# Performance work log

Hardware: AMD Instinct MI355X
Metric: run time of the kernel (lower is better)

The kernel has to match this reference:

```python
import jax, jax.numpy as jnp
import numpy as np

T, NC, NT, D, H, LBL = 8, 512, 512, 256, 8, 3
NBF = 1419  # performer default: int(256 * ln(256))
EPS = 1e-4


def setup_inputs() -> dict:
    key = jax.random.key(0)
    ks = jax.random.split(key, 16)
    rn = lambda i, shape, sc=1.0: jax.random.normal(ks[i], shape, dtype=jnp.float32) * sc
    w = 1.0 / np.sqrt(D)
    return {
        'x_ctx': rn(0, (T, NC, D)),
        'label_train': rn(1, (T, NC, LBL)),
        'x_tgt': rn(2, (T, NT, D)),
        # task_encoder: 3-layer MLP (256+label_dim -> 256 -> 256 -> 256), ReLU
        'W1': rn(3, (D + LBL, D), 1.0 / np.sqrt(D + LBL)), 'b1': jnp.zeros((D,), jnp.float32),
        'W2': rn(4, (D, D), w), 'b2': jnp.zeros((D,), jnp.float32),
        'W3': rn(5, (D, D), w), 'b3': jnp.zeros((D,), jnp.float32),
        # per-head projections (8 distinct 256->256 Linears each for k/v/q)
        'Wk': rn(6, (H, D, D), w), 'bk': jnp.zeros((H, D), jnp.float32),
        'Wv': rn(7, (H, D, D), w), 'bv': jnp.zeros((H, D), jnp.float32),
        'Wq': rn(8, (H, D, D), w), 'bq': jnp.zeros((H, D), jnp.float32),
        # output head-merge projection (8*256 -> 256) and mu (256 -> 256)
        'Wo': rn(9, (H * D, D), 1.0 / np.sqrt(H * D)), 'bo': jnp.zeros((D,), jnp.float32),
        'Wmu': rn(10, (D, D), w), 'bmu': jnp.zeros((D,), jnp.float32),
        # FAVOR+ random projection matrix [nb_features, dim_head]
        'proj': rn(11, (NBF, D)),
    }


def _softmax_kernel(data, proj, is_query):
    # Performer FAVOR+ positive softmax-kernel features. data: [t,h,n,d]
    dn = D ** -0.25
    ratio = NBF ** -0.5
    dd = jnp.einsum('thnd,fd->thnf', data * dn, proj)          # [t,h,n,F]
    diag = 0.5 * jnp.sum(data * data, axis=-1) * (dn * dn)      # [t,h,n]
    if is_query:
        m = jnp.max(dd, axis=-1, keepdims=True)
    else:
        m = jnp.max(dd, axis=(-2, -1), keepdims=True)
    return ratio * (jnp.exp(dd - diag[..., None] - m) + EPS)


def reference(x_ctx, label_train, x_tgt, W1, b1, W2, b2, W3, b3,
              Wk, bk, Wv, bv, Wq, bq, Wo, bo, Wmu, bmu, proj):
    # task_encoder MLP on [x_ctx, label]
    h = jax.nn.relu(jnp.concatenate([x_ctx, label_train], axis=-1) @ W1 + b1)
    h = jax.nn.relu(h @ W2 + b2)
    cf = jax.nn.relu(h @ W3 + b3)                               # context_features [t,Nc,D]
    # per-head full-width projections: k from x_ctx, v from context_features, q from x_tgt
    k = jnp.einsum('tnd,hde->thne', x_ctx, Wk) + bk[None, :, None, :]
    v = jnp.einsum('tnd,hde->thne', cf, Wv) + bv[None, :, None, :]
    q = jnp.einsum('tnd,hde->thne', x_tgt, Wq) + bq[None, :, None, :]
    # non-causal Performer linear attention
    qp = _softmax_kernel(q, proj, True)                         # [t,h,Nt,F]
    kp = _softmax_kernel(k, proj, False)                        # [t,h,Nc,F]
    ksum = jnp.sum(kp, axis=-2)                                 # [t,h,F]
    d_inv = 1.0 / jnp.einsum('thnf,thf->thn', qp, ksum)         # [t,h,Nt]
    ctx = jnp.einsum('thnf,thne->thfe', kp, v)                  # [t,h,F,D]
    out = jnp.einsum('thnf,thfe,thn->thne', qp, ctx, d_inv)     # [t,h,Nt,D]
    # torch: permute(0,2,3,1).view(t,Nt,-1) -> head index fastest-varying
    out = jnp.transpose(out, (0, 2, 3, 1)).reshape(out.shape[0], out.shape[2], -1)
    rep = out @ Wo + bo                                         # [t,Nt,D]
    return rep @ Wmu + bmu                                      # mu / sample_features
```

## Files before the change

### kernel.cpp

```cpp
#include <hip/hip_runtime.h>
#include <hip/hip_bf16.h>

typedef __hip_bfloat16 bf16;
typedef __attribute__((ext_vector_type(8))) short short8;
typedef __attribute__((ext_vector_type(4))) float f32x4;
typedef __attribute__((ext_vector_type(4))) unsigned short us4;
#define DEV __device__ __forceinline__

static constexpr int T_ = 8, NC = 512, NT = 512, D_ = 256, H_ = 8, NBF = 1419;
static constexpr int FT32 = 46;
static constexpr float EPS_ = 1e-4f;
static constexpr float DN = 0.25f;
static constexpr float DIAG_SC = 0.03125f;

DEV float bf2f(unsigned short u) { return __uint_as_float(((unsigned)u) << 16); }
DEV float tofloat(bf16 x) { return __bfloat162float(x); }
DEV unsigned short f2bu(float x) { bf16 h = __float2bfloat16(x); return *(unsigned short*)&h; }

DEV float ldx(const void* p, long i, int isb) {
  if (isb) return bf2f(((const unsigned short*)p)[i]);
  return ((const float*)p)[i];
}
DEV void stx(void* p, long i, float v, int isb) {
  if (isb) ((bf16*)p)[i] = __float2bfloat16(v);
  else     ((float*)p)[i] = v;
}

DEV void async_copy16(const void* g, void* lds) {
  __builtin_amdgcn_global_load_lds(
      (const __attribute__((address_space(1))) unsigned int*)g,
      (__attribute__((address_space(3))) unsigned int*)lds, 16, 0, 0);
}

__global__ __launch_bounds__(256)
void detect_dtype(const void* __restrict__ x, int* __restrict__ flag)
{
  __shared__ int bad;
  if (threadIdx.x == 0) bad = 0;
  __syncthreads();
  int mybad = 0;
  for (int j = 0; j < 16; j++) {
    long i = 2L * (threadIdx.x + 256L * j);
    unsigned short u = ((const unsigned short*)x)[i];
    int e = (u >> 7) & 0xff, mant = u & 0x7f;
    bool b = (e == 0xff) || (e >= 141) || (e <= 93 && !(e == 0 && mant == 0));
    mybad += b ? 1 : 0;
  }
  atomicAdd(&bad, mybad);
  __syncthreads();
  if (threadIdx.x == 0) *flag = (bad > 1024) ? 0 : 1;
}

__global__ __launch_bounds__(256)
void conv_proj(const void* __restrict__ proj, bf16* __restrict__ projB,
               const int* __restrict__ dtFlag)
{
  const int fl = *dtFlag;
  int f = blockIdx.x, t = threadIdx.x;
  float v = (f < NBF) ? ldx(proj, (long)f * 256 + t, fl) : 0.f;
  projB[(long)f * 256 + t] = __float2bfloat16(v);
}

__global__ __launch_bounds__(256)
void conv_bf16(const void* __restrict__ src, bf16* __restrict__ dst,
               const int* __restrict__ dtFlag)
{
  const int fl = *dtFlag;
  long i = (long)blockIdx.x * 256 + threadIdx.x;
  dst[i] = __float2bfloat16(ldx(src, i, fl));
}

__global__ __launch_bounds__(256)
void conv_wT(const void* __restrict__ Wk, const void* __restrict__ Wv,
             const void* __restrict__ Wq, const void* __restrict__ Wo,
             const void* __restrict__ W1, const void* __restrict__ W2,
             const void* __restrict__ W3, const void* __restrict__ Wmu,
             bf16* __restrict__ WkT, bf16* __restrict__ WvT,
             bf16* __restrict__ WqT, bf16* __restrict__ WoT,
             bf16* __restrict__ W1T, bf16* __restrict__ W2T,
             bf16* __restrict__ W3T, bf16* __restrict__ WmuT,
             const int* __restrict__ dtFlag)
{
  __shared__ float tile[32][33];
  const int fl = *dtFlag;
  const int kt = blockIdx.x, nt = blockIdx.y, z = blockIdx.z, t = threadIdx.x;
  const void* in; bf16* out; int K; int perm = 0; long off = 0;
  if (z < 8)        { in = Wk;  out = WkT;  K = 256; off = (long)z * 65536; }
  else if (z < 16)  { in = Wv;  out = WvT;  K = 256; off = (long)(z - 8) * 65536; }
  else if (z < 24)  { in = Wq;  out = WqT;  K = 256; off = (long)(z - 16) * 65536; }
  else if (z == 24) { in = Wo;  out = WoT;  K = 2048; perm = 1; }
  else if (z == 25) { in = W1;  out = W1T;  K = 256; }
  else if (z == 26) { in = W2;  out = W2T;  K = 256; }
  else if (z == 27) { in = W3;  out = W3T;  K = 256; }
  else              { in = Wmu; out = WmuT; K = 256; }
  if (K == 256 && kt >= 8) return;
  const int k0 = kt * 32, n0 = nt * 32;
  const int row = t >> 3, cb = (t & 7) * 4;
  {
    int kk = k0 + row;
    int krow = perm ? (((kk & 255) << 3) | (kk >> 8)) : kk;
#pragma unroll
    for (int j = 0; j < 4; j++)
      tile[row][cb + j] = ldx(in, off + (long)krow * 256 + n0 + cb + j, fl);
  }
  __syncthreads();
  us4 o;
#pragma unroll
  for (int j = 0; j < 4; j++) o[j] = f2bu(tile[cb + j][row]);
  *(us4*)(out + off + (long)(n0 + row) * K + k0 + cb) = o;
}

__global__ __launch_bounds__(256)
void init_zero(float* __restrict__ p)
{
  p[blockIdx.x * 256 + threadIdx.x] = 0.f;
}

__global__ __launch_bounds__(256)
void gemm_mfma(const bf16* __restrict__ A, const bf16* __restrict__ BT,
               const void* __restrict__ bias,
               void* __restrict__ C, int cMode, int epi, int cT,
               const int* __restrict__ dtFlag, float* __restrict__ diagOut,
               float* __restrict__ svOut,
               int M, int N, int K, long sA, int divA, long sB, int modB, long sBias)
{
  __shared__ alignas(16) bf16 As[2][64 * 64];
  __shared__ alignas(16) bf16 Bs[2][64 * 64];
  const int fl = *dtFlag;
  const int cB = (cMode == 2) ? fl : cMode;
  const int t = threadIdx.x;
  const int bz = blockIdx.z;
  const long aOff = (long)(bz / divA) * sA;
  const long bOff = (long)(bz % modB) * sB;
  const long biasOff = (long)(bz % modB) * sBias;
  const long cOff = (long)bz * (long)M * N;
  const int m0 = blockIdx.y * 64, n0 = blockIdx.x * 64;
  const int w = t >> 6, l = t & 63, quad = l >> 4, ln = l & 15;
  const bf16* Ab = A + aOff + (long)m0 * K;
  const bf16* Bb = BT + bOff + (long)n0 * K;
  const int srow = l >> 3;
  const int scc = (l & 7) ^ srow;
  f32x4 acc[4] = {};

  auto stage = [&](int buf, int k0) {
#pragma unroll
    for (int j = 0; j < 2; j++) {
      const int rbase = 32 * j + 8 * w;
      const int row = rbase + srow;
      async_copy16(Ab + (long)row * K + k0 + scc * 8, &As[buf][rbase * 64]);
      async_copy16(Bb + (long)row * K + k0 + scc * 8, &Bs[buf][rbase * 64]);
    }
  };

  stage(0, 0);
  __syncthreads();

  int cur = 0;
  for (int k0 = 0; k0 < K; k0 += 64) {
    if (k0 + 64 < K) stage(cur ^ 1, k0 + 64);
    const bf16* Ac = &As[cur][0];
    const bf16* Bc = &Bs[cur][0];
    const int arow = 16 * w + ln;
#pragma unroll
    for (int ks = 0; ks < 2; ks++) {
      short8 a = *(const short8*)(Ac + arow * 64 + (((ks * 4 + quad) ^ (arow & 7)) << 3));
#pragma unroll
      for (int i = 0; i < 4; i++) {
        const int brow = 16 * i + ln;
        short8 b = *(const short8*)(Bc + brow * 64 + (((ks * 4 + quad) ^ (brow & 7)) << 3));
        acc[i] = __builtin_amdgcn_mfma_f32_16x16x32_bf16(a, b, acc[i], 0, 0, 0);
      }
    }
    asm volatile("s_waitcnt vmcnt(0)" ::: "memory");
    __builtin_amdgcn_s_barrier();
    __builtin_amdgcn_sched_barrier(0);
    cur ^= 1;
  }

  float s2[4] = {0.f, 0.f, 0.f, 0.f};
  if (cT == 2) {
    const int mm = m0 + 16 * w + quad * 4;
    const int tile = mm >> 5, off = mm & 31;
#pragma unroll
    for (int i = 0; i < 4; i++) {
      int n = n0 + 16 * i + ln;
      us4 cv;
      float colsum = 0.f;
#pragma unroll
      for (int r = 0; r < 4; r++) {
        float c = acc[i][r];
        if (epi >= 1) c += ldx(bias, biasOff + n, fl);
        if (epi == 2) c = fmaxf(c, 0.f);
        colsum += c;
        cv[r] = f2bu(c);
      }
      *(us4*)((bf16*)C + cOff + ((long)tile * N + n) * 32 + off) = cv;
      if (svOut) {
        colsum += __shfl_xor(colsum, 16);
        colsum += __shfl_xor(colsum, 32);
        if (quad == 0) atomicAdd(&svOut[(long)bz * N + n], colsum);
      }
    }
  } else {
#pragma unroll
    for (int i = 0; i < 4; i++) {
#pragma unroll
      for (int r = 0; r < 4; r++) {
        int m = m0 + 16 * w + quad * 4 + r;
        int n = n0 + 16 * i + ln;
        float c = acc[i][r];
        if (epi >= 1) c += ldx(bias, biasOff + n, fl);
        if (epi == 2) c = fmaxf(c, 0.f);
        s2[r] += c * c;
        stx(C, cOff + (long)m * N + n, c, cB);
      }
    }
  }
  if (diagOut) {
#pragma unroll
    for (int r = 0; r < 4; r++) {
      float s = s2[r];
      s += __shfl_xor(s, 1); s += __shfl_xor(s, 2);
      s += __shfl_xor(s, 4); s += __shfl_xor(s, 8);
      if (ln == 0)
        atomicAdd(&diagOut[(long)bz * M + m0 + 16 * w + quad * 4 + r], DIAG_SC * s);
    }
  }
}

__global__ __launch_bounds__(256)
void gemm_mfma32v2(const bf16* __restrict__ A, const bf16* __restrict__ BT,
                   const void* __restrict__ bias,
                   void* __restrict__ C, int cMode, int epi,
                   const int* __restrict__ dtFlag, int M, int N, int K)
{
  __shared__ alignas(16) bf16 As[2][32 * 64];
  __shared__ alignas(16) bf16 Bs[2][64 * 64];
  const int fl = *dtFlag;
  const int cB = (cMode == 2) ? fl : cMode;
  const int t = threadIdx.x;
  const int m0 = blockIdx.y * 32, n0 = blockIdx.x * 64;
  const int w = t >> 6, l = t & 63, quad = l >> 4, ln = l & 15;
  const int mi = w & 1, nh = w >> 1;
  const bf16* Ab = A + (long)m0 * K;
  const bf16* Bb = BT + (long)n0 * K;
  const int srow = l >> 3;
  const int scc = (l & 7) ^ srow;
  f32x4 acc[2] = {};

  auto stage = [&](int buf, int k0) {
    async_copy16(Ab + (long)(8 * w + srow) * K + k0 + scc * 8, &As[buf][(8 * w) * 64]);
#pragma unroll
    for (int j = 0; j < 2; j++) {
      const int rbase = 32 * j + 8 * w;
      async_copy16(Bb + (long)(rbase + srow) * K + k0 + scc * 8, &Bs[buf][rbase * 64]);
    }
  };

  stage(0, 0);
  __syncthreads();

  int cur = 0;
  for (int k0 = 0; k0 < K; k0 += 64) {
    if (k0 + 64 < K) stage(cur ^ 1, k0 + 64);
    const bf16* Ac = &As[cur][0];
    const bf16* Bc = &Bs[cur][0];
    const int arow = 16 * mi + ln;
#pragma unroll
    for (int ks = 0; ks < 2; ks++) {
      short8 a = *(const short8*)(Ac + arow * 64 + (((ks * 4 + quad) ^ (arow & 7)) << 3));
#pragma unroll
      for (int i = 0; i < 2; i++) {
        const int brow = 16 * (2 * nh + i) + ln;
        short8 b = *(const short8*)(Bc + brow * 64 + (((ks * 4 + quad) ^ (brow & 7)) << 3));
        acc[i] = __builtin_amdgcn_mfma_f32_16x16x32_bf16(a, b, acc[i], 0, 0, 0);
      }
    }
    asm volatile("s_waitcnt vmcnt(0)" ::: "memory");
    __builtin_amdgcn_s_barrier();
    __builtin_amdgcn_sched_barrier(0);
    cur ^= 1;
  }

#pragma unroll
  for (int i = 0; i < 2; i++) {
#pragma unroll
    for (int r = 0; r < 4; r++) {
      int m = m0 + 16 * mi + quad * 4 + r;
      int n = n0 + 16 * (2 * nh + i) + ln;
      float c = acc[i][r];
      if (epi >= 1) c += ldx(bias, n, fl);
      if (epi == 2) c = fmaxf(c, 0.f);
      stx(C, (long)m * N + n, c, cB);
    }
  }
}

__global__ __launch_bounds__(256)
void gemm_wo_splitk(const bf16* __restrict__ A, const bf16* __restrict__ BT,
                    float* __restrict__ P, int M, int N, int K)
{
  __shared__ alignas(16) bf16 As[2][64 * 64];
  __shared__ alignas(16) bf16 Bs[2][64 * 64];
  const int t = threadIdx.x;
  const int z = blockIdx.z;
  const int m0 = blockIdx.y * 64, n0 = blockIdx.x * 64;
  const int w = t >> 6, l = t & 63, quad = l >> 4, ln = l & 15;
  const bf16* Ab = A + (long)m0 * K;
  const bf16* Bb = BT + (long)n0 * K;
  const int srow = l >> 3, scc = (l & 7) ^ srow;
  f32x4 acc[4] = {};
  const int kbase = z * 1024, kend = kbase + 1024;

  auto stage = [&](int buf, int k0) {
#pragma unroll
    for (int j = 0; j < 2; j++) {
      const int rbase = 32 * j + 8 * w;
      const int row = rbase + srow;
      async_copy16(Ab + (long)row * K + k0 + scc * 8, &As[buf][rbase * 64]);
      async_copy16(Bb + (long)row * K + k0 + scc * 8, &Bs[buf][rbase * 64]);
    }
  };

  stage(0, kbase);
  __syncthreads();

  int cur = 0;
  for (int k0 = kbase; k0 < kend; k0 += 64) {
    if (k0 + 64 < kend) stage(cur ^ 1, k0 + 64);
    const bf16* Ac = &As[cur][0];
    const bf16* Bc = &Bs[cur][0];
    const int arow = 16 * w + ln;
#pragma unroll
    for (int ks = 0; ks < 2; ks++) {
      short8 a = *(const short8*)(Ac + arow * 64 + (((ks * 4 + quad) ^ (arow & 7)) << 3));
#pragma unroll
      for (int i = 0; i < 4; i++) {
        const int brow = 16 * i + ln;
        short8 b = *(const short8*)(Bc + brow * 64 + (((ks * 4 + quad) ^ (brow & 7)) << 3));
        acc[i] = __builtin_amdgcn_mfma_f32_16x16x32_bf16(a, b, acc[i], 0, 0, 0);
      }
    }
    asm volatile("s_waitcnt vmcnt(0)" ::: "memory");
    __builtin_amdgcn_s_barrier();
    __builtin_amdgcn_sched_barrier(0);
    cur ^= 1;
  }

  float* Pz = P + (long)z * M * N;
#pragma unroll
  for (int i = 0; i < 4; i++) {
#pragma unroll
    for (int r = 0; r < 4; r++) {
      int m = m0 + 16 * w + quad * 4 + r;
      int n = n0 + 16 * i + ln;
      Pz[(long)m * N + n] = acc[i][r];
    }
  }
}

__global__ __launch_bounds__(256)
void reduce_partials(const float* __restrict__ P, const void* __restrict__ bo,
                     bf16* __restrict__ rep, const int* __restrict__ dtFlag)
{
  const int fl = *dtFlag;
  long idx = (long)blockIdx.x * 256 + threadIdx.x;
  int n = idx & 255;
  float s = ldx(bo, n, fl) + P[idx] + P[1048576 + idx];
  rep[idx] = __float2bfloat16(s);
}

__global__ __launch_bounds__(256)
void fixup_h1(bf16* __restrict__ h1, const void* __restrict__ label,
              const void* __restrict__ W1, const void* __restrict__ b1,
              const int* __restrict__ dtFlag)
{
  const int fl = *dtFlag;
  int idx = blockIdx.x * 256 + threadIdx.x;
  int m = idx >> 8, n = idx & 255;
  float c = tofloat(h1[idx]) + ldx(b1, n, fl);
#pragma unroll
  for (int j = 0; j < 3; j++)
    c += ldx(label, m * 3 + j, fl) * ldx(W1, (256 + j) * 256 + n, fl);
  h1[idx] = __float2bfloat16(fmaxf(c, 0.f));
}

__global__ __launch_bounds__(256)
void key_fused_mfma(const bf16* __restrict__ k, const bf16* __restrict__ vQ,
                    const bf16* __restrict__ projB, const float* __restrict__ diagk,
                    float* __restrict__ ksumE, bf16* __restrict__ ctxQ,
                    float* __restrict__ mpart, float* __restrict__ csRp,
                    float* __restrict__ ktotp)
{
  __shared__ alignas(16) bf16 kS[3][32 * 256];
  __shared__ alignas(16) bf16 pS[2][64 * 40];
  __shared__ float wredM[4];
  __shared__ float wredK[4];

  const int bz = blockIdx.x, ft = blockIdx.y, f0 = ft * 64;
  const int t = threadIdx.x;
  const int w = t >> 6, l = t & 63, quad = l >> 4, ln = l & 15;
  const int fmine = f0 + 16 * w + ln;
  const bool fv = fmine < NBF;

  const bf16* kb = k + (long)bz * NC * 256;
  const bf16* vqb = vQ + (long)bz * 16 * 256 * 32;
  const float* db = diagk + bz * NC;

  auto stage = [&](int buf, int n0) {
#pragma unroll
    for (int j = 0; j < 4; j++) {
      int row = w * 8 + j * 2 + (l >> 5);
      int cc = (l & 31) ^ ((2 * j + (l >> 5)) & 7);
      async_copy16(kb + (long)(n0 + row) * 256 + cc * 8,
                   &kS[buf][w * 2048 + j * 512]);
    }
  };
  stage(0, 0);
  stage(1, 32);

  short8 pf[8];
  {
    const bf16* prow = projB + (long)fmine * 256;
#pragma unroll
    for (int kc = 0; kc < 8; kc++)
      pf[kc] = *(const short8*)(prow + kc * 32 + quad * 8);
  }

  f32x4 acc[4][4] = {};
  float ksumP = 0.f, mP = -1e30f;

  __syncthreads();

  int cur = 0;
  for (int it = 0; it < 16; it++) {
    const int n0 = it * 32;
    short8 bfr[4];
#pragma unroll
    for (int ei = 0; ei < 4; ei++) {
      int e = 64 * w + 16 * ei + ln;
      bfr[ei] = *(const short8*)(vqb + ((long)it * 256 + e) * 32 + quad * 8);
    }
    f32x4 dv0 = *(const f32x4*)(db + n0 + quad * 4);
    f32x4 dv1 = *(const f32x4*)(db + n0 + 16 + quad * 4);
    __builtin_amdgcn_sched_barrier(0);
    if (it + 2 < 16) {
      int nb = cur + 2; if (nb >= 3) nb -= 3;
      stage(nb, n0 + 64);
    }
    __builtin_amdgcn_sched_barrier(0);

    const bf16* kcur = &kS[cur][0];
    f32x4 dd[2][2] = {};
    __builtin_amdgcn_s_setprio(1);
#pragma unroll
    for (int kc = 0; kc < 8; kc++) {
      const int hf = kc & 1;
#pragma unroll
      for (int mi = 0; mi < 2; mi++) {
        short8 a = *(const short8*)(kcur + (16 * mi + ln) * 256 +
                                    (((kc * 4 + quad) ^ (ln & 7)) << 3));
        dd[mi][hf] = __builtin_amdgcn_mfma_f32_16x16x32_bf16(a, pf[kc], dd[mi][hf], 0, 0, 0);
      }
    }
    __builtin_amdgcn_s_setprio(0);
    bf16* pcur = &pS[it & 1][0];
#pragma unroll
    for (int mi = 0; mi < 2; mi++) {
      us4 ev;
      f32x4 dvv = mi ? dv1 : dv0;
#pragma unroll
      for (int r = 0; r < 4; r++) {
        float sc = DN * (dd[mi][0][r] + dd[mi][1][r]);
        float E = fv ? __expf(fminf(sc - dvv[r], 80.f)) : 0.f;
        unsigned short u = f2bu(E);
        ksumP += bf2f(u);
        if (fv) mP = fmaxf(mP, sc);
        ev[r] = u;
      }
      *(us4*)(pcur + (16 * w + ln) * 40 + 16 * mi + quad * 4) = ev;
    }
    asm volatile("s_waitcnt vmcnt(4) lgkmcnt(0)" ::: "memory");
    __builtin_amdgcn_s_barrier();
    __builtin_amdgcn_sched_barrier(0);

    __builtin_amdgcn_s_setprio(1);
#pragma unroll
    for (int fh = 0; fh < 4; fh++) {
      short8 a = *(const short8*)(pcur + (16 * fh + ln) * 40 + quad * 8);
#pragma unroll
      for (int ei = 0; ei < 4; ei++)
        acc[fh][ei] = __builtin_amdgcn_mfma_f32_16x16x32_bf16(a, bfr[ei], acc[fh][ei], 0, 0, 0);
    }
    __builtin_amdgcn_s_setprio(0);
    cur = (cur == 2) ? 0 : cur + 1;
  }
  __syncthreads();

#pragma unroll
  for (int fh = 0; fh < 4; fh++) {
    const int ft32 = 2 * ft + (fh >> 1);
    const int f32b = 16 * (fh & 1) + quad * 4;
#pragma unroll
    for (int ei = 0; ei < 4; ei++) {
      int e = 64 * w + 16 * ei + ln;
      us4 cv;
#pragma unroll
      for (int r = 0; r < 4; r++) cv[r] = f2bu(acc[fh][ei][r]);
      *(us4*)(&ctxQ[((long)(bz * FT32 + ft32) * 256 + e) * 32 + f32b]) = cv;
    }
  }

#pragma unroll
  for (int ei = 0; ei < 4; ei++) {
    float col = 0.f;
#pragma unroll
    for (int fh = 0; fh < 4; fh++)
#pragma unroll
      for (int r = 0; r < 4; r++) col += acc[fh][ei][r];
    col += __shfl_xor(col, 16);
    col += __shfl_xor(col, 32);
    if (quad == 0)
      csRp[((long)bz * 23 + ft) * 256 + 64 * w + 16 * ei + ln] = col;
  }

  float s = ksumP;
  s += __shfl_xor(s, 16); s += __shfl_xor(s, 32);
  if (quad == 0 && fv) ksumE[(long)bz * NBF + fmine] = s;
  float s2 = s;
  s2 += __shfl_xor(s2, 1); s2 += __shfl_xor(s2, 2);
  s2 += __shfl_xor(s2, 4); s2 += __shfl_xor(s2, 8);
  if (l == 0) wredK[w] = s2;

  float m = mP;
#pragma unroll
  for (int off = 1; off < 64; off <<= 1) m = fmaxf(m, __shfl_xor(m, off));
  if (l == 0) wredM[w] = m;
  __syncthreads();
  if (t == 0) {
    mpart[bz * 23 + ft] = fmaxf(fmaxf(wredM[0], wredM[1]), fmaxf(wredM[2], wredM[3]));
    ktotp[bz * 23 + ft] = wredK[0] + wredK[1] + wredK[2] + wredK[3];
  }
}

__global__ __launch_bounds__(256)
void finalize_red(const float* __restrict__ mpart, const float* __restrict__ csRp,
                  const float* __restrict__ ktotp, float* __restrict__ mk,
                  float* __restrict__ csR, float* __restrict__ ktotR)
{
  int bz = blockIdx.x, t = threadIdx.x;
  float s = 0.f;
  for (int ft = 0; ft < 23; ft++)
    s += csRp[((long)bz * 23 + ft) * 256 + t];
  csR[bz * 256 + t] = s;
  int w = t >> 6, l = t & 63;
  if (w == 0) {
    float m = (l < 23) ? mpart[bz * 23 + l] : -1e30f;
#pragma unroll
    for (int off = 32; off > 0; off >>= 1) m = fmaxf(m, __shfl_down(m, off));
    if (l == 0) mk[bz] = m;
  } else if (w == 1) {
    float kk = (l < 23) ? ktotp[bz * 23 + l] : 0.f;
#pragma unroll
    for (int off = 32; off > 0; off >>= 1) kk += __shfl_down(kk, off);
    if (l == 0) ktotR[bz] = kk;
  }
}

__global__ __launch_bounds__(256)
void q_fused_mfma(const bf16* __restrict__ q, const bf16* __restrict__ projB,
                  const float* __restrict__ diagq, const bf16* __restrict__ ctxQ,
                  const float* __restrict__ ksum, const float* __restrict__ Sv,
                  const float* __restrict__ csR, const float* __restrict__ ktotR,
                  const float* __restrict__ mk, bf16* __restrict__ merged)
{
  __shared__ alignas(16) bf16 projS[2][32 * 256];
  __shared__ alignas(16) bf16 eS[64 * 40];
  __shared__ float dS[64];
  __shared__ float svS[256];
  __shared__ float crS[256];
  __shared__ float sS[64];
  __shared__ float mS[64];
  __shared__ float seS[64];

  const int bz = blockIdx.x, nt = blockIdx.y, t = threadIdx.x;
  const int w = t >> 6, l = t & 63, quad = l >> 4, ln = l & 15;
  const int tq = bz / H_, hh = bz % H_;
  const bf16* cqb = ctxQ + (long)bz * FT32 * 256 * 32;
  const bf16* qb = q + ((long)bz * NT + nt * 64) * 256;
  const float emk = __expf(-mk[bz]);

  auto stage_proj = [&](int buf, int f0n) {
#pragma unroll
    for (int j = 0; j < 4; j++) {
      int row = 8 * w + 2 * j + (l >> 5);
      int cc = (l & 31) ^ (row & 7);
      async_copy16(projB + (long)(f0n + row) * 256 + cc * 8,
                   &projS[buf][(8 * w + 2 * j) * 256]);
    }
  };
  stage_proj(0, 0);

  short8 qf[8];
  {
    const bf16* qrow = qb + (long)(16 * w + ln) * 256;
#pragma unroll
    for (int kc = 0; kc < 8; kc++)
      qf[kc] = *(const short8*)(qrow + kc * 32 + quad * 8);
  }
  if (t < 64) dS[t] = diagq[(long)bz * NT + nt * 64 + t];
  svS[t] = Sv[bz * 256 + t];
  crS[t] = csR[bz * 256 + t];

  f32x4 acc[4][4] = {};
  float sPart[4] = {0.f, 0.f, 0.f, 0.f};
  float sEp[4] = {0.f, 0.f, 0.f, 0.f};
  float mPart[4] = {0.f, 0.f, 0.f, 0.f};
  __syncthreads();

  for (int ft = 0; ft < FT32; ft++) {
    const int f0 = ft * 32;
    const bf16* pcur = &projS[ft & 1][0];
    short8 cfr[4];
#pragma unroll
    for (int i = 0; i < 4; i++) {
      int e = 16 * (4 * w + i) + ln;
      cfr[i] = *(const short8*)(cqb + ((long)ft * 256 + e) * 32 + quad * 8);
    }
    const float kv0 = (f0 + ln < NBF) ? ksum[(long)bz * NBF + f0 + ln] : 0.f;
    const float kv1 = (f0 + 16 + ln < NBF) ? ksum[(long)bz * NBF + f0 + 16 + ln] : 0.f;
    if (ft + 1 < FT32) stage_proj((ft + 1) & 1, f0 + 32);

    f32x4 dd0 = {}, dd1 = {};
#pragma unroll
    for (int kc = 0; kc < 8; kc++) {
      const int co = ((kc * 4 + quad) ^ (ln & 7)) << 3;
      short8 b0 = *(const short8*)(pcur + ln * 256 + co);
      dd0 = __builtin_amdgcn_mfma_f32_16x16x32_bf16(qf[kc], b0, dd0, 0, 0, 0);
      short8 b1 = *(const short8*)(pcur + (16 + ln) * 256 + co);
      dd1 = __builtin_amdgcn_mfma_f32_16x16x32_bf16(qf[kc], b1, dd1, 0, 0, 0);
    }
    const bool fv0 = (f0 + ln) < NBF;
    const bool fv1 = (f0 + 16 + ln) < NBF;
#pragma unroll
    for (int r = 0; r < 4; r++) {
      float E0 = fv0 ? __expf(fminf(DN * dd0[r], 80.f)) : 0.f;
      float E1 = fv1 ? __expf(fminf(DN * dd1[r], 80.f)) : 0.f;
      bf16 h0 = __float2bfloat16(E0), h1v = __float2bfloat16(E1);
      float e0 = tofloat(h0), e1 = tofloat(h1v);
      eS[(16 * w + quad * 4 + r) * 40 + ln] = h0;
      eS[(16 * w + quad * 4 + r) * 40 + 16 + ln] = h1v;
      sPart[r] += e0 * kv0 + e1 * kv1;
      sEp[r] += e0 + e1;
      mPart[r] = fmaxf(mPart[r], fmaxf(e0, e1));
    }
    asm volatile("s_waitcnt lgkmcnt(0)" ::: "memory");
    __builtin_amdgcn_s_barrier();
    __builtin_amdgcn_sched_barrier(0);

#pragma unroll
    for (int mh = 0; mh < 4; mh++) {
      short8 a = *(const short8*)(&eS[(16 * mh + ln) * 40 + quad * 8]);
#pragma unroll
      for (int i = 0; i < 4; i++)
        acc[mh][i] = __builtin_amdgcn_mfma_f32_16x16x32_bf16(a, cfr[i], acc[mh][i], 0, 0, 0);
    }
    asm volatile("s_waitcnt vmcnt(0) lgkmcnt(0)" ::: "memory");
    __builtin_amdgcn_s_barrier();
    __builtin_amdgcn_sched_barrier(0);
  }
  __syncthreads();

#pragma unroll
  for (int r = 0; r < 4; r++) {
    float s = sPart[r], m = mPart[r], se = sEp[r];
#pragma unroll
    for (int off = 1; off < 16; off <<= 1) {
      s += __shfl_xor(s, off);
      m = fmaxf(m, __shfl_xor(m, off));
      se += __shfl_xor(se, off);
    }
    if (ln == 0) {
      sS[16 * w + quad * 4 + r] = s;
      mS[16 * w + quad * 4 + r] = m;
      seS[16 * w + quad * 4 + r] = se;
    }
  }
  __syncthreads();

  const float ktotv = ktotR[bz];
#pragma unroll
  for (int mh = 0; mh < 4; mh++) {
#pragma unroll
    for (int r = 0; r < 4; r++) {
      int row = 16 * mh + quad * 4 + r;
      float st = sS[row];
      float se = seS[row];
      float mt = fmaxf(mS[row], 1e-30f);
      float c = __expf(-dS[row]) / mt;
      float A = c * se + (float)NBF * EPS_;
      float den = emk * (c * st + EPS_ * ktotv) + (float)NC * EPS_ * A;
      float inv = 1.f / den;
#pragma unroll
      for (int i = 0; i < 4; i++) {
        int e = 16 * (4 * w + i) + ln;
        float val = (emk * (c * acc[mh][i][r] + EPS_ * crS[e]) + EPS_ * svS[e] * A) * inv;
        merged[((long)tq * NT + nt * 64 + row) * 2048 + hh * 256 + e] =
            __float2bfloat16(val);
      }
    }
  }
}

extern "C" void kernel_launch(void* const* d_in, const int* in_sizes, int n_in,
                              void* d_out, int out_size, void* d_ws, size_t ws_size,
                              hipStream_t stream)
{
  const void* x_ctx = d_in[0];
  const void* label = d_in[1];
  const void* x_tgt = d_in[2];
  const void* W1 = d_in[3];
  const void* b1 = d_in[4];
  const void* W2 = d_in[5];
  const void* b2 = d_in[6];
  const void* W3 = d_in[7];
  const void* b3 = d_in[8];
  const void* Wk = d_in[9];
  const void* bk = d_in[10];
  const void* Wv = d_in[11];
  const void* bv = d_in[12];
  const void* Wq = d_in[13];
  const void* bq = d_in[14];
  const void* Wo = d_in[15];
  const void* bo = d_in[16];
  const void* Wmu = d_in[17];
  const void* bmu = d_in[18];
  const void* proj = d_in[19];

  float* W = (float*)d_ws;
  const long F0 = 0, F1 = 4194304, F2 = 8388608;
  const long CTXQ_F = (long)64 * FT32 * 256 * 32 / 2;
  const long F3 = F2 + CTXQ_F;
  bf16* kB = (bf16*)(W + F0);
  bf16* qB = (bf16*)(W + F0);
  bf16* rep = (bf16*)(W + F0);
  bf16* vQ = (bf16*)(W + F1);
  bf16* merged = (bf16*)(W + F1);
  bf16* xtB = (bf16*)(W + F1);
  bf16* h1 = (bf16*)(W + F2);
  bf16* h2 = (bf16*)(W + F2 + 524288);
  bf16* cf = (bf16*)(W + F2 + 1048576);
  bf16* xcB = (bf16*)(W + F2 + 1572864);
  bf16* ctxQ = (bf16*)(W + F2);
  float* woP = W + F2;
  long o = F3;
  auto alloc = [&](long n) { float* p = W + o; o += n; return p; };
  float* zbase = W + o;
  float* dgk = alloc(32768);
  float* dgq = alloc(32768);
  float* Sv = alloc(64 * 256);
  float* csR = alloc(64 * 256);
  float* ktotR = alloc(64);
  alloc(192);
  float* ksumE = alloc((long)64 * NBF);
  float* mpart = alloc(64 * 23);
  float* mk = alloc(64);
  int* dtFlag = (int*)alloc(64);
  float* csRp = alloc((long)64 * 23 * 256);
  float* ktotp = alloc(64 * 23);
  bf16* projB = (bf16*)alloc((long)FT32 * 32 * 256 / 2);
  bf16* WkT = (bf16*)alloc(262144);
  bf16* WvT = (bf16*)alloc(262144);
  bf16* WqT = (bf16*)alloc(262144);
  bf16* WoT = (bf16*)alloc(262144);
  bf16* W1T = (bf16*)alloc(32768);
  bf16* W2T = (bf16*)alloc(32768);
  bf16* W3T = (bf16*)alloc(32768);
  bf16* WmuT = (bf16*)alloc(32768);
  (void)ws_size; (void)in_sizes; (void)n_in; (void)out_size;

  const dim3 B(256);
  detect_dtype<<<1, B, 0, stream>>>(x_ctx, dtFlag);
  conv_proj<<<FT32 * 32, B, 0, stream>>>(proj, projB, dtFlag);
  conv_wT<<<dim3(64, 8, 29), B, 0, stream>>>(Wk, Wv, Wq, Wo, W1, W2, W3, Wmu,
                                             WkT, WvT, WqT, WoT, W1T, W2T, W3T, WmuT, dtFlag);
  conv_bf16<<<4096, B, 0, stream>>>(x_ctx, xcB, dtFlag);
  init_zero<<<320, B, 0, stream>>>(zbase);
  gemm_mfma32v2<<<dim3(4, 128), B, 0, stream>>>(
      xcB, W1T, nullptr, h1, 1, 0, dtFlag, 4096, 256, 256);
  fixup_h1<<<4096, B, 0, stream>>>(h1, label, W1, b1, dtFlag);
  gemm_mfma32v2<<<dim3(4, 128), B, 0, stream>>>(
      h1, W2T, b2, h2, 1, 2, dtFlag, 4096, 256, 256);
  gemm_mfma32v2<<<dim3(4, 128), B, 0, stream>>>(
      h2, W3T, b3, cf, 1, 2, dtFlag, 4096, 256, 256);
  gemm_mfma<<<dim3(4, 8, 64), B, 0, stream>>>(
      xcB, WkT, bk, kB, 1, 1, 0, dtFlag, dgk, nullptr,
      512, 256, 256, 131072L, 8, 65536L, 8, 256L);
  gemm_mfma<<<dim3(4, 8, 64), B, 0, stream>>>(
      cf, WvT, bv, vQ, 1, 1, 2, dtFlag, nullptr, Sv,
      512, 256, 256, 131072L, 8, 65536L, 8, 256L);
  key_fused_mfma<<<dim3(64, 23), B, 0, stream>>>(kB, vQ, projB, dgk, ksumE, ctxQ,
                                                 mpart, csRp, ktotp);
  finalize_red<<<64, B, 0, stream>>>(mpart, csRp, ktotp, mk, csR, ktotR);
  conv_bf16<<<4096, B, 0, stream>>>(x_tgt, xtB, dtFlag);
  gemm_mfma<<<dim3(4, 8, 64), B, 0, stream>>>(
      xtB, WqT, bq, qB, 1, 1, 0, dtFlag, dgq, nullptr,
      512, 256, 256, 131072L, 8, 65536L, 8, 256L);
  q_fused_mfma<<<dim3(64, 8), B, 0, stream>>>(qB, projB, dgq, ctxQ, ksumE,
                                              Sv, csR, ktotR, mk, merged);
  gemm_wo_splitk<<<dim3(4, 64, 2), B, 0, stream>>>(merged, WoT, woP, 4096, 256, 2048);
  reduce_partials<<<4096, B, 0, stream>>>(woP, bo, rep, dtFlag);
  gemm_mfma32v2<<<dim3(4, 128), B, 0, stream>>>(
      rep, WmuT, bmu, d_out, 2, 1, dtFlag, 4096, 256, 256);
}
```

Before: 387.7 us.

## Fuse prep kernels, fold label fixup into GEMM epilogue, deepen q-kernel pipeline

Merges the weight transpose, proj conversion, x_ctx conversion and zero-init kernels into one launch. Folds the label·W1 term, bias and ReLU of the first MLP layer into the GEMM epilogue, removing the fixup pass over h1. Makes the query feature kernel use triple-buffered proj staging and double-buffered exponent tiles, dropping a per-iteration barrier and raising MFMA priority. The reduced synchronization relies on correct vmcnt counts and buffer reuse distances.

```diff
diff --git a/kernel.cpp b/kernel.cpp
--- a/kernel.cpp
+++ b/kernel.cpp
@@ -52,16 +52,6 @@
 }
 
 __global__ __launch_bounds__(256)
-void conv_proj(const void* __restrict__ proj, bf16* __restrict__ projB,
-               const int* __restrict__ dtFlag)
-{
-  const int fl = *dtFlag;
-  int f = blockIdx.x, t = threadIdx.x;
-  float v = (f < NBF) ? ldx(proj, (long)f * 256 + t, fl) : 0.f;
-  projB[(long)f * 256 + t] = __float2bfloat16(v);
-}
-
-__global__ __launch_bounds__(256)
 void conv_bf16(const void* __restrict__ src, bf16* __restrict__ dst,
                const int* __restrict__ dtFlag)
 {
@@ -71,19 +61,45 @@
 }
 
 __global__ __launch_bounds__(256)
-void conv_wT(const void* __restrict__ Wk, const void* __restrict__ Wv,
-             const void* __restrict__ Wq, const void* __restrict__ Wo,
-             const void* __restrict__ W1, const void* __restrict__ W2,
-             const void* __restrict__ W3, const void* __restrict__ Wmu,
-             bf16* __restrict__ WkT, bf16* __restrict__ WvT,
-             bf16* __restrict__ WqT, bf16* __restrict__ WoT,
-             bf16* __restrict__ W1T, bf16* __restrict__ W2T,
-             bf16* __restrict__ W3T, bf16* __restrict__ WmuT,
-             const int* __restrict__ dtFlag)
+void prep_all(const void* __restrict__ Wk, const void* __restrict__ Wv,
+              const void* __restrict__ Wq, const void* __restrict__ Wo,
+              const void* __restrict__ W1, const void* __restrict__ W2,
+              const void* __restrict__ W3, const void* __restrict__ Wmu,
+              const void* __restrict__ proj, const void* __restrict__ x_ctx,
+              bf16* __restrict__ WkT, bf16* __restrict__ WvT,
+              bf16* __restrict__ WqT, bf16* __restrict__ WoT,
+              bf16* __restrict__ W1T, bf16* __restrict__ W2T,
+              bf16* __restrict__ W3T, bf16* __restrict__ WmuT,
+              bf16* __restrict__ projB, bf16* __restrict__ xcB,
+              float* __restrict__ zbase, const int* __restrict__ dtFlag)
 {
   __shared__ float tile[32][33];
   const int fl = *dtFlag;
   const int kt = blockIdx.x, nt = blockIdx.y, z = blockIdx.z, t = threadIdx.x;
+
+  if (z == 29) {
+    int b = nt * 64 + kt;
+#pragma unroll
+    for (int r = 0; r < 3; r++) {
+      int f = b * 3 + r;
+      if (f < FT32 * 32) {
+        float v = (f < NBF) ? ldx(proj, (long)f * 256 + t, fl) : 0.f;
+        projB[(long)f * 256 + t] = __float2bfloat16(v);
+      }
+    }
+    return;
+  }
+  if (z == 30) {
+    int b = nt * 64 + kt;
+#pragma unroll
+    for (int j = 0; j < 8; j++) {
+      long i = (long)b * 2048 + j * 256 + t;
+      xcB[i] = __float2bfloat16(ldx(x_ctx, i, fl));
+    }
+    if (b < 320) zbase[b * 256 + t] = 0.f;
+    return;
+  }
+
   const void* in; bf16* out; int K; int perm = 0; long off = 0;
   if (z < 8)        { in = Wk;  out = WkT;  K = 256; off = (long)z * 65536; }
   else if (z < 16)  { in = Wv;  out = WvT;  K = 256; off = (long)(z - 8) * 65536; }
@@ -108,12 +124,6 @@
 #pragma unroll
   for (int j = 0; j < 4; j++) o[j] = f2bu(tile[cb + j][row]);
   *(us4*)(out + off + (long)(n0 + row) * K + k0 + cb) = o;
-}
-
-__global__ __launch_bounds__(256)
-void init_zero(float* __restrict__ p)
-{
-  p[blockIdx.x * 256 + threadIdx.x] = 0.f;
 }
 
 __global__ __launch_bounds__(256)
@@ -232,7 +242,8 @@
 void gemm_mfma32v2(const bf16* __restrict__ A, const bf16* __restrict__ BT,
                    const void* __restrict__ bias,
                    void* __restrict__ C, int cMode, int epi,
-                   const int* __restrict__ dtFlag, int M, int N, int K)
+                   const int* __restrict__ dtFlag, int M, int N, int K,
+                   const void* __restrict__ labp, const void* __restrict__ labW)
 {
   __shared__ alignas(16) bf16 As[2][32 * 64];
   __shared__ alignas(16) bf16 Bs[2][64 * 64];
@@ -290,6 +301,11 @@
       int n = n0 + 16 * (2 * nh + i) + ln;
       float c = acc[i][r];
       if (epi >= 1) c += ldx(bias, n, fl);
+      if (labp) {
+#pragma unroll
+        for (int j = 0; j < 3; j++)
+          c += ldx(labp, (long)m * 3 + j, fl) * ldx(labW, (long)(256 + j) * 256 + n, fl);
+      }
       if (epi == 2) c = fmaxf(c, 0.f);
       stx(C, (long)m * N + n, c, cB);
     }
@@ -371,21 +387,6 @@
 }
 
 __global__ __launch_bounds__(256)
-void fixup_h1(bf16* __restrict__ h1, const void* __restrict__ label,
-              const void* __restrict__ W1, const void* __restrict__ b1,
-              const int* __restrict__ dtFlag)
-{
-  const int fl = *dtFlag;
-  int idx = blockIdx.x * 256 + threadIdx.x;
-  int m = idx >> 8, n = idx & 255;
-  float c = tofloat(h1[idx]) + ldx(b1, n, fl);
-#pragma unroll
-  for (int j = 0; j < 3; j++)
-    c += ldx(label, m * 3 + j, fl) * ldx(W1, (256 + j) * 256 + n, fl);
-  h1[idx] = __float2bfloat16(fmaxf(c, 0.f));
-}
-
-__global__ __launch_bounds__(256)
 void key_fused_mfma(const bf16* __restrict__ k, const bf16* __restrict__ vQ,
                     const bf16* __restrict__ projB, const float* __restrict__ diagk,
                     float* __restrict__ ksumE, bf16* __restrict__ ctxQ,
@@ -574,8 +575,8 @@
                   const float* __restrict__ csR, const float* __restrict__ ktotR,
                   const float* __restrict__ mk, bf16* __restrict__ merged)
 {
-  __shared__ alignas(16) bf16 projS[2][32 * 256];
-  __shared__ alignas(16) bf16 eS[64 * 40];
+  __shared__ alignas(16) bf16 projS[3][32 * 256];
+  __shared__ alignas(16) bf16 eS[2][64 * 40];
   __shared__ float dS[64];
   __shared__ float svS[256];
   __shared__ float crS[256];
@@ -600,6 +601,7 @@
     }
   };
   stage_proj(0, 0);
+  stage_proj(1, 32);
 
   short8 qf[8];
   {
@@ -618,9 +620,10 @@
   float mPart[4] = {0.f, 0.f, 0.f, 0.f};
   __syncthreads();
 
+  int cur = 0;
   for (int ft = 0; ft < FT32; ft++) {
     const int f0 = ft * 32;
-    const bf16* pcur = &projS[ft & 1][0];
+    const bf16* pcur = &projS[cur][0];
     short8 cfr[4];
 #pragma unroll
     for (int i = 0; i < 4; i++) {
@@ -629,9 +632,15 @@
     }
     const float kv0 = (f0 + ln < NBF) ? ksum[(long)bz * NBF + f0 + ln] : 0.f;
     const float kv1 = (f0 + 16 + ln < NBF) ? ksum[(long)bz * NBF + f0 + 16 + ln] : 0.f;
-    if (ft + 1 < FT32) stage_proj((ft + 1) & 1, f0 + 32);
+    __builtin_amdgcn_sched_barrier(0);
+    if (ft + 2 < FT32) {
+      int nb = cur + 2; if (nb >= 3) nb -= 3;
+      stage_proj(nb, f0 + 64);
+    }
+    __builtin_amdgcn_sched_barrier(0);
 
     f32x4 dd0 = {}, dd1 = {};
+    __builtin_amdgcn_s_setprio(1);
 #pragma unroll
     for (int kc = 0; kc < 8; kc++) {
       const int co = ((kc * 4 + quad) ^ (ln & 7)) << 3;
@@ -640,34 +649,36 @@
       short8 b1 = *(const short8*)(pcur + (16 + ln) * 256 + co);
       dd1 = __builtin_amdgcn_mfma_f32_16x16x32_bf16(qf[kc], b1, dd1, 0, 0, 0);
     }
+    __builtin_amdgcn_s_setprio(0);
     const bool fv0 = (f0 + ln) < NBF;
     const bool fv1 = (f0 + 16 + ln) < NBF;
+    bf16* ecur = &eS[ft & 1][0];
 #pragma unroll
     for (int r = 0; r < 4; r++) {
       float E0 = fv0 ? __expf(fminf(DN * dd0[r], 80.f)) : 0.f;
       float E1 = fv1 ? __expf(fminf(DN * dd1[r], 80.f)) : 0.f;
       bf16 h0 = __float2bfloat16(E0), h1v = __float2bfloat16(E1);
       float e0 = tofloat(h0), e1 = tofloat(h1v);
-      eS[(16 * w + quad * 4 + r) * 40 + ln] = h0;
-      eS[(16 * w + quad * 4 + r) * 40 + 16 + ln] = h1v;
+      ecur[(16 * w + quad * 4 + r) * 40 + ln] = h0;
+      ecur[(16 * w + quad * 4 + r) * 40 + 16 + ln] = h1v;
       sPart[r] += e0 * kv0 + e1 * kv1;
       sEp[r] += e0 + e1;
       mPart[r] = fmaxf(mPart[r], fmaxf(e0, e1));
     }
-    asm volatile("s_waitcnt lgkmcnt(0)" ::: "memory");
+    asm volatile("s_waitcnt vmcnt(4) lgkmcnt(0)" ::: "memory");
     __builtin_amdgcn_s_barrier();
     __builtin_amdgcn_sched_barrier(0);
 
+    __builtin_amdgcn_s_setprio(1);
 #pragma unroll
     for (int mh = 0; mh < 4; mh++) {
-      short8 a = *(const short8*)(&eS[(16 * mh + ln) * 40 + quad * 8]);
+      short8 a = *(const short8*)(ecur + (16 * mh + ln) * 40 + quad * 8);
 #pragma unroll
       for (int i = 0; i < 4; i++)
         acc[mh][i] = __builtin_amdgcn_mfma_f32_16x16x32_bf16(a, cfr[i], acc[mh][i], 0, 0, 0);
     }
-    asm volatile("s_waitcnt vmcnt(0) lgkmcnt(0)" ::: "memory");
-    __builtin_amdgcn_s_barrier();
-    __builtin_amdgcn_sched_barrier(0);
+    __builtin_amdgcn_s_setprio(0);
+    cur = (cur == 2) ? 0 : cur + 1;
   }
   __syncthreads();
 
@@ -781,18 +792,15 @@
 
   const dim3 B(256);
   detect_dtype<<<1, B, 0, stream>>>(x_ctx, dtFlag);
-  conv_proj<<<FT32 * 32, B, 0, stream>>>(proj, projB, dtFlag);
-  conv_wT<<<dim3(64, 8, 29), B, 0, stream>>>(Wk, Wv, Wq, Wo, W1, W2, W3, Wmu,
-                                             WkT, WvT, WqT, WoT, W1T, W2T, W3T, WmuT, dtFlag);
-  conv_bf16<<<4096, B, 0, stream>>>(x_ctx, xcB, dtFlag);
-  init_zero<<<320, B, 0, stream>>>(zbase);
+  prep_all<<<dim3(64, 8, 31), B, 0, stream>>>(
+      Wk, Wv, Wq, Wo, W1, W2, W3, Wmu, proj, x_ctx,
+      WkT, WvT, WqT, WoT, W1T, W2T, W3T, WmuT, projB, xcB, zbase, dtFlag);
   gemm_mfma32v2<<<dim3(4, 128), B, 0, stream>>>(
-      xcB, W1T, nullptr, h1, 1, 0, dtFlag, 4096, 256, 256);
-  fixup_h1<<<4096, B, 0, stream>>>(h1, label, W1, b1, dtFlag);
+      xcB, W1T, b1, h1, 1, 2, dtFlag, 4096, 256, 256, label, W1);
   gemm_mfma32v2<<<dim3(4, 128), B, 0, stream>>>(
-      h1, W2T, b2, h2, 1, 2, dtFlag, 4096, 256, 256);
+      h1, W2T, b2, h2, 1, 2, dtFlag, 4096, 256, 256, nullptr, nullptr);
   gemm_mfma32v2<<<dim3(4, 128), B, 0, stream>>>(
-      h2, W3T, b3, cf, 1, 2, dtFlag, 4096, 256, 256);
+      h2, W3T, b3, cf, 1, 2, dtFlag, 4096, 256, 256, nullptr, nullptr);
   gemm_mfma<<<dim3(4, 8, 64), B, 0, stream>>>(
       xcB, WkT, bk, kB, 1, 1, 0, dtFlag, dgk, nullptr,
       512, 256, 256, 131072L, 8, 65536L, 8, 256L);
@@ -811,5 +819,5 @@
   gemm_wo_splitk<<<dim3(4, 64, 2), B, 0, stream>>>(merged, WoT, woP, 4096, 256, 2048);
   reduce_partials<<<4096, B, 0, stream>>>(woP, bo, rep, dtFlag);
   gemm_mfma32v2<<<dim3(4, 128), B, 0, stream>>>(
-      rep, WmuT, bmu, d_out, 2, 1, dtFlag, 4096, 256, 256);
-}
+      rep, WmuT, bmu, d_out, 2, 1, dtFlag, 4096, 256, 256, nullptr, nullptr);
+}
```

Result: faster. 376.7 us (-2.8%).
